# Kernel optimization log

Hardware: AMD Instinct MI355X
Metric: run time of the kernel (lower is better)

Reference implementation:

```python
import jax, jax.numpy as jnp
import numpy as np

N_EMBD = 1024
N_HEAD = 16
HEAD_SIZE = N_EMBD // N_HEAD  # 64
EPS = 1e-5


def layer_norm(x, gamma, beta):
    mu = jnp.mean(x, axis=-1, keepdims=True)
    var = jnp.var(x, axis=-1, keepdims=True)
    return (x - mu) * jax.lax.rsqrt(var + EPS) * gamma + beta


def setup_inputs() -> dict:
    key = jax.random.key(0)
    ks = jax.random.split(key, 12)
    B, T, C, H, hs = 4, 2048, N_EMBD, N_HEAD, HEAD_SIZE
    s = 0.02
    return {
        "x": jax.random.normal(ks[0], (B, T, C), jnp.float32),
        # per-head projections, stacked over heads: [H, C, hs]
        "Wq": jax.random.normal(ks[1], (H, C, hs), jnp.float32) * s,
        "Wk": jax.random.normal(ks[2], (H, C, hs), jnp.float32) * s,
        "Wv": jax.random.normal(ks[3], (H, C, hs), jnp.float32) * s,
        "Wo": jax.random.normal(ks[4], (C, C), jnp.float32) * s,
        "bo": jnp.zeros((C,), jnp.float32),
        "W1": jax.random.normal(ks[5], (C, 4 * C), jnp.float32) * s,
        "b1": jnp.zeros((4 * C,), jnp.float32),
        "W2": jax.random.normal(ks[6], (4 * C, C), jnp.float32) * s,
        "b2": jnp.zeros((C,), jnp.float32),
        "g1": jnp.ones((C,), jnp.float32),
        "be1": jnp.zeros((C,), jnp.float32),
        "g2": jnp.ones((C,), jnp.float32),
        "be2": jnp.zeros((C,), jnp.float32),
    }


def reference(x, Wq, Wk, Wv, Wo, bo, W1, b1, W2, b2, g1, be1, g2, be2):
    B, T, C = x.shape
    # --- self-attention branch (pre-LN) ---
    h = layer_norm(x, g1, be1)
    q = jnp.einsum("btc,hcd->bhtd", h, Wq)
    k = jnp.einsum("btc,hcd->bhtd", h, Wk)
    v = jnp.einsum("btc,hcd->bhtd", h, Wv)
    scale = HEAD_SIZE ** -0.5
    wei = jnp.einsum("bhtd,bhsd->bhts", q, k) * scale  # [B,H,T,T]
    causal = jnp.tril(jnp.ones((T, T), bool))
    wei = jnp.where(causal, wei, -jnp.inf)
    wei = jax.nn.softmax(wei, axis=-1)
    attn = jnp.einsum("bhts,bhsd->bhtd", wei, v)  # [B,H,T,hs]
    # concat heads -> [B,T,C]
    attn = attn.transpose(0, 2, 1, 3).reshape(B, T, C)
    x = x + attn @ Wo + bo
    # --- MLP branch (pre-LN) ---
    h = layer_norm(x, g2, be2)
    h = jax.nn.relu(h @ W1 + b1) @ W2 + b2
    return x + h
```

## Files before the change

### kernel.cpp

```cpp
#include <hip/hip_runtime.h>
#include <cstdint>
#include <cstddef>


typedef unsigned short u16;
typedef __attribute__((ext_vector_type(8))) __bf16 bf16x8;
typedef __attribute__((ext_vector_type(4))) short s16x4;
typedef __attribute__((ext_vector_type(4))) float f32x4;

#if defined(__has_builtin)
#if __has_builtin(__builtin_amdgcn_global_load_lds)
#define HAS_GLL 1
#endif
#endif

#define QSCALE 0.18033688011112042f

__device__ __forceinline__ u16 f2bf(float f) {
  union { float f; unsigned int u; } c; c.f = f;
  unsigned int u = c.u;
  u += 0x7FFFu + ((u >> 16) & 1u);
  return (u16)(u >> 16);
}
__device__ __forceinline__ u16 f2bf_fast(float f) {
  union { float f; unsigned int u; } c; c.f = f;
  return (u16)((c.u + 0x8000u) >> 16);
}

__device__ __forceinline__ float fexp2(float x) {
#if defined(__HIP_DEVICE_COMPILE__)
#if defined(__has_builtin) && __has_builtin(__builtin_amdgcn_exp2f)
  return __builtin_amdgcn_exp2f(x);
#else
  float r;
  asm("v_exp_f32 %0, %1" : "=v"(r) : "v"(x));
  return r;
#endif
#else
  return x;
#endif
}

__device__ __forceinline__ f32x4 mfma_pv(s16x4 a, s16x4 b, f32x4 c) {
#if defined(__HIP_DEVICE_COMPILE__)
#if defined(__has_builtin) && __has_builtin(__builtin_amdgcn_mfma_f32_16x16x16bf16_1k)
  return __builtin_amdgcn_mfma_f32_16x16x16bf16_1k(a, b, c, 0, 0, 0);
#else
  f32x4 d;
  asm volatile("v_mfma_f32_16x16x16_bf16 %0, %1, %2, %3"
               : "=v"(d) : "v"(a), "v"(b), "v"(c));
  return d;
#endif
#else
  (void)a; (void)b;
  return c;
#endif
}

__device__ __forceinline__ void stage16(const u16* g, u16* l, int lane) {
#ifdef HAS_GLL
  __builtin_amdgcn_global_load_lds(
      (const __attribute__((address_space(1))) uint32_t*)(g),
      (__attribute__((address_space(3))) uint32_t*)(l), 16, 0, 0);
#else
  *(int4*)(l + lane * 8) = *(const int4*)g;
#endif
}

__global__ __launch_bounds__(256) void ln_k(const float* __restrict__ x,
                                            const float* __restrict__ g,
                                            const float* __restrict__ be,
                                            u16* __restrict__ out) {
  const int row = blockIdx.x;
  const int t = threadIdx.x;
  const float4 v = ((const float4*)(x + (size_t)row * 1024))[t];
  float s = v.x + v.y + v.z + v.w;
  float s2 = v.x * v.x + v.y * v.y + v.z * v.z + v.w * v.w;
#pragma unroll
  for (int off = 32; off > 0; off >>= 1) {
    s += __shfl_down(s, off);
    s2 += __shfl_down(s2, off);
  }
  __shared__ float red[8];
  if ((t & 63) == 0) { red[t >> 6] = s; red[4 + (t >> 6)] = s2; }
  __syncthreads();
  const float ts = red[0] + red[1] + red[2] + red[3];
  const float ts2 = red[4] + red[5] + red[6] + red[7];
  const float mu = ts * (1.0f / 1024.0f);
  const float var = ts2 * (1.0f / 1024.0f) - mu * mu;
  const float rstd = rsqrtf(var + 1e-5f);
  const float4 gv = ((const float4*)g)[t];
  const float4 bv = ((const float4*)be)[t];
  u16* op = out + (size_t)row * 1024 + t * 4;
  op[0] = f2bf((v.x - mu) * rstd * gv.x + bv.x);
  op[1] = f2bf((v.y - mu) * rstd * gv.y + bv.y);
  op[2] = f2bf((v.z - mu) * rstd * gv.z + bv.z);
  op[3] = f2bf((v.w - mu) * rstd * gv.w + bv.w);
}

__global__ __launch_bounds__(256) void transpose_k(const float* __restrict__ in,
                                                   u16* __restrict__ out,
                                                   int R, int Cc) {
  __shared__ float tile[32][33];
  const size_t base = (size_t)blockIdx.z * R * Cc;
  const int r0 = blockIdx.x * 32, c0 = blockIdx.y * 32;
  const int tx = threadIdx.x & 31, ty = threadIdx.x >> 5;
  const float* ip = in + base;
  u16* op = out + base;
#pragma unroll
  for (int i = 0; i < 32; i += 8)
    tile[ty + i][tx] = ip[(size_t)(r0 + ty + i) * Cc + c0 + tx];
  __syncthreads();
#pragma unroll
  for (int i = 0; i < 32; i += 8)
    op[(size_t)(c0 + ty + i) * R + r0 + tx] = f2bf(tile[tx][ty + i]);
}

template <int MODE>
__global__ __launch_bounds__(256, 2) void gemm_k(
    const u16* __restrict__ A, const u16* __restrict__ Bt,
    const float* __restrict__ bias, const float* __restrict__ resid,
    void* __restrict__ out0, void* __restrict__ out1, void* __restrict__ out2,
    int M, int N, int K) {
  __shared__ u16 As[2][2][128 * 32];
  __shared__ u16 Bs[2][2][128 * 32];
  const int tid = threadIdx.x;
  const int lane = tid & 63;
  const int w = tid >> 6;
  const int wm = w & 1, wn = w >> 1;
  const int l15 = lane & 15, lq = lane >> 4;
  const int m0 = blockIdx.x * 128, n0 = blockIdx.y * 128;
  const int srow = lane >> 2, scol = (lane & 3) * 8;

  f32x4 acc[4][4] = {};

  const u16* gA0 = A  + (size_t)(m0 + w * 32 + srow) * K + scol;
  const u16* gA1 = gA0 + (size_t)16 * K;
  const u16* gB0 = Bt + (size_t)(n0 + w * 32 + srow) * K + scol;
  const u16* gB1 = gB0 + (size_t)16 * K;
  const int lofs = (w * 32) * 32;

  auto STAGE = [&](int buf, int k0) {
    stage16(gA0 + k0,      &As[buf][0][lofs], lane);
    stage16(gA1 + k0,      &As[buf][0][lofs + 512], lane);
    stage16(gA0 + k0 + 32, &As[buf][1][lofs], lane);
    stage16(gA1 + k0 + 32, &As[buf][1][lofs + 512], lane);
    stage16(gB0 + k0,      &Bs[buf][0][lofs], lane);
    stage16(gB1 + k0,      &Bs[buf][0][lofs + 512], lane);
    stage16(gB0 + k0 + 32, &Bs[buf][1][lofs], lane);
    stage16(gB1 + k0 + 32, &Bs[buf][1][lofs + 512], lane);
  };

  STAGE(0, 0);

  int cur = 0;
  for (int k0 = 0; k0 < K; k0 += 64) {
    if (k0 + 64 < K) {
      STAGE(cur ^ 1, k0 + 64);
      asm volatile("s_waitcnt vmcnt(8)" ::: "memory");
    } else {
      asm volatile("s_waitcnt vmcnt(0)" ::: "memory");
    }
    __builtin_amdgcn_s_barrier();
    __builtin_amdgcn_sched_barrier(0);
#pragma unroll
    for (int kk = 0; kk < 2; ++kk) {
      bf16x8 af[4], bfr[4];
#pragma unroll
      for (int i = 0; i < 4; ++i)
        af[i] = *(const bf16x8*)&As[cur][kk][(wm * 64 + i * 16 + l15) * 32 + lq * 8];
#pragma unroll
      for (int j = 0; j < 4; ++j)
        bfr[j] = *(const bf16x8*)&Bs[cur][kk][(wn * 64 + j * 16 + l15) * 32 + lq * 8];
#pragma unroll
      for (int i = 0; i < 4; ++i)
#pragma unroll
        for (int j = 0; j < 4; ++j)
          acc[i][j] = __builtin_amdgcn_mfma_f32_16x16x32_bf16(af[i], bfr[j], acc[i][j], 0, 0, 0);
    }
    __builtin_amdgcn_sched_barrier(0);
    __builtin_amdgcn_s_barrier();
    cur ^= 1;
  }

#pragma unroll
  for (int i = 0; i < 4; ++i) {
    const int mbase = m0 + wm * 64 + i * 16 + lq * 4;
#pragma unroll
    for (int j = 0; j < 4; ++j) {
      const int ncol = n0 + wn * 64 + j * 16 + l15;
#pragma unroll
      for (int r = 0; r < 4; ++r) {
        const float v = acc[i][j][r];
        const int m = mbase + r;
        if (MODE == 0) {
          const int which = ncol >> 10;
          const int hh = (ncol >> 6) & 15;
          const int dd = ncol & 63;
          const int tt = m & 2047;
          const size_t bhb = (size_t)((m >> 11) * 16 + hh) * 131072;
          if (which == 0) {
            ((u16*)out0)[bhb + tt * 64 + dd] = f2bf(v * QSCALE);
          } else if (which == 1) {
            ((u16*)out1)[bhb + (tt >> 4) * 1024 + (dd >> 5) * 512 +
                         ((((dd & 31) >> 3) * 16 + (tt & 15)) << 3) + (dd & 7)] = f2bf(v);
          } else {
            ((u16*)out2)[bhb + (dd >> 4) * 32768 + (tt >> 4) * 256 +
                         (((dd & 15) + (((tt >> 2) & 3)) * 16) << 2) + (tt & 3)] = f2bf(v);
          }
        } else if (MODE == 1 || MODE == 3) {
          ((float*)out0)[(size_t)m * N + ncol] =
              v + bias[ncol] + resid[(size_t)m * N + ncol];
        } else {
          const float t2 = v + bias[ncol];
          ((u16*)out0)[(size_t)m * N + ncol] = f2bf(t2 > 0.0f ? t2 : 0.0f);
        }
      }
    }
  }
}

__global__ __launch_bounds__(256, 4) void flash_k(const u16* __restrict__ q,
                                                  const u16* __restrict__ k,
                                                  const u16* __restrict__ vt,
                                                  u16* __restrict__ attn) {
  const int bh = blockIdx.x;
  const int qblk = 15 - blockIdx.y;
  const int bb = bh >> 4, hh = bh & 15;
  const int tid = threadIdx.x;
  const int lane = tid & 63, wid = tid >> 6;
  const int l15 = lane & 15, lq = lane >> 4;
  const int q0w = qblk * 128 + wid * 32;

  const u16* qrowA = q + ((size_t)bh * 2048 + q0w + l15) * 64 + lq * 8;
  const bf16x8 qA0 = *(const bf16x8*)qrowA;
  const bf16x8 qA1 = *(const bf16x8*)(qrowA + 32);
  const u16* qrowB = qrowA + 16 * 64;
  const bf16x8 qB0 = *(const bf16x8*)qrowB;
  const bf16x8 qB1 = *(const bf16x8*)(qrowB + 32);

  const u16* kC = k + (size_t)bh * 131072 + lane * 8;
  const u16* vC = vt + (size_t)bh * 131072 + lane * 4;

  f32x4 oA[4] = {}, oB[4] = {};
  float lA = 0.0f, lB = 0.0f;

  const int nt = q0w >> 4;

#pragma unroll 2
  for (int t = 0; t < nt; ++t) {
    const int ko = t * 1024, vo = t * 256;
    const bf16x8 ck0 = *(const bf16x8*)(kC + ko);
    const bf16x8 ck1 = *(const bf16x8*)(kC + ko + 512);
    const s16x4 cv0 = *(const s16x4*)(vC + vo);
    const s16x4 cv1 = *(const s16x4*)(vC + vo + 32768);
    const s16x4 cv2 = *(const s16x4*)(vC + vo + 65536);
    const s16x4 cv3 = *(const s16x4*)(vC + vo + 98304);

    f32x4 stA = {}, stB = {};
    __builtin_amdgcn_s_setprio(1);
    stA = __builtin_amdgcn_mfma_f32_16x16x32_bf16(ck0, qA0, stA, 0, 0, 0);
    stA = __builtin_amdgcn_mfma_f32_16x16x32_bf16(ck1, qA1, stA, 0, 0, 0);
    stB = __builtin_amdgcn_mfma_f32_16x16x32_bf16(ck0, qB0, stB, 0, 0, 0);
    stB = __builtin_amdgcn_mfma_f32_16x16x32_bf16(ck1, qB1, stB, 0, 0, 0);
    __builtin_amdgcn_s_setprio(0);

    const float a0 = fexp2(stA[0]), a1 = fexp2(stA[1]);
    const float a2 = fexp2(stA[2]), a3 = fexp2(stA[3]);
    const float b0 = fexp2(stB[0]), b1 = fexp2(stB[1]);
    const float b2 = fexp2(stB[2]), b3 = fexp2(stB[3]);
    lA += (a0 + a1) + (a2 + a3);
    lB += (b0 + b1) + (b2 + b3);
    s16x4 pfA, pfB;
    pfA[0] = (short)f2bf_fast(a0); pfA[1] = (short)f2bf_fast(a1);
    pfA[2] = (short)f2bf_fast(a2); pfA[3] = (short)f2bf_fast(a3);
    pfB[0] = (short)f2bf_fast(b0); pfB[1] = (short)f2bf_fast(b1);
    pfB[2] = (short)f2bf_fast(b2); pfB[3] = (short)f2bf_fast(b3);

    __builtin_amdgcn_s_setprio(1);
    oA[0] = mfma_pv(cv0, pfA, oA[0]);
    oA[1] = mfma_pv(cv1, pfA, oA[1]);
    oA[2] = mfma_pv(cv2, pfA, oA[2]);
    oA[3] = mfma_pv(cv3, pfA, oA[3]);
    oB[0] = mfma_pv(cv0, pfB, oB[0]);
    oB[1] = mfma_pv(cv1, pfB, oB[1]);
    oB[2] = mfma_pv(cv2, pfB, oB[2]);
    oB[3] = mfma_pv(cv3, pfB, oB[3]);
    __builtin_amdgcn_s_setprio(0);
  }

  {
    const int ko = nt * 1024, vo = nt * 256;
    const bf16x8 ck0 = *(const bf16x8*)(kC + ko);
    const bf16x8 ck1 = *(const bf16x8*)(kC + ko + 512);
    const s16x4 cv0 = *(const s16x4*)(vC + vo);
    const s16x4 cv1 = *(const s16x4*)(vC + vo + 32768);
    const s16x4 cv2 = *(const s16x4*)(vC + vo + 65536);
    const s16x4 cv3 = *(const s16x4*)(vC + vo + 98304);

    f32x4 stA = {}, stB = {};
    stA = __builtin_amdgcn_mfma_f32_16x16x32_bf16(ck0, qA0, stA, 0, 0, 0);
    stA = __builtin_amdgcn_mfma_f32_16x16x32_bf16(ck1, qA1, stA, 0, 0, 0);
    stB = __builtin_amdgcn_mfma_f32_16x16x32_bf16(ck0, qB0, stB, 0, 0, 0);
    stB = __builtin_amdgcn_mfma_f32_16x16x32_bf16(ck1, qB1, stB, 0, 0, 0);
#pragma unroll
    for (int r = 0; r < 4; ++r)
      if (lq * 4 + r > l15) stA[r] = -1e30f;

    const float a0 = fexp2(stA[0]), a1 = fexp2(stA[1]);
    const float a2 = fexp2(stA[2]), a3 = fexp2(stA[3]);
    const float b0 = fexp2(stB[0]), b1 = fexp2(stB[1]);
    const float b2 = fexp2(stB[2]), b3 = fexp2(stB[3]);
    lA += (a0 + a1) + (a2 + a3);
    lB += (b0 + b1) + (b2 + b3);
    s16x4 pfA, pfB;
    pfA[0] = (short)f2bf_fast(a0); pfA[1] = (short)f2bf_fast(a1);
    pfA[2] = (short)f2bf_fast(a2); pfA[3] = (short)f2bf_fast(a3);
    pfB[0] = (short)f2bf_fast(b0); pfB[1] = (short)f2bf_fast(b1);
    pfB[2] = (short)f2bf_fast(b2); pfB[3] = (short)f2bf_fast(b3);

    oA[0] = mfma_pv(cv0, pfA, oA[0]);
    oA[1] = mfma_pv(cv1, pfA, oA[1]);
    oA[2] = mfma_pv(cv2, pfA, oA[2]);
    oA[3] = mfma_pv(cv3, pfA, oA[3]);
    oB[0] = mfma_pv(cv0, pfB, oB[0]);
    oB[1] = mfma_pv(cv1, pfB, oB[1]);
    oB[2] = mfma_pv(cv2, pfB, oB[2]);
    oB[3] = mfma_pv(cv3, pfB, oB[3]);
  }

  {
    const int ko = (nt + 1) * 1024, vo = (nt + 1) * 256;
    const bf16x8 ck0 = *(const bf16x8*)(kC + ko);
    const bf16x8 ck1 = *(const bf16x8*)(kC + ko + 512);
    const s16x4 cv0 = *(const s16x4*)(vC + vo);
    const s16x4 cv1 = *(const s16x4*)(vC + vo + 32768);
    const s16x4 cv2 = *(const s16x4*)(vC + vo + 65536);
    const s16x4 cv3 = *(const s16x4*)(vC + vo + 98304);

    f32x4 stB = {};
    stB = __builtin_amdgcn_mfma_f32_16x16x32_bf16(ck0, qB0, stB, 0, 0, 0);
    stB = __builtin_amdgcn_mfma_f32_16x16x32_bf16(ck1, qB1, stB, 0, 0, 0);
#pragma unroll
    for (int r = 0; r < 4; ++r)
      if (lq * 4 + r > l15) stB[r] = -1e30f;

    const float b0 = fexp2(stB[0]), b1 = fexp2(stB[1]);
    const float b2 = fexp2(stB[2]), b3 = fexp2(stB[3]);
    lB += (b0 + b1) + (b2 + b3);
    s16x4 pfB;
    pfB[0] = (short)f2bf_fast(b0); pfB[1] = (short)f2bf_fast(b1);
    pfB[2] = (short)f2bf_fast(b2); pfB[3] = (short)f2bf_fast(b3);

    oB[0] = mfma_pv(cv0, pfB, oB[0]);
    oB[1] = mfma_pv(cv1, pfB, oB[1]);
    oB[2] = mfma_pv(cv2, pfB, oB[2]);
    oB[3] = mfma_pv(cv3, pfB, oB[3]);
  }

  lA += __shfl_xor(lA, 16);
  lA += __shfl_xor(lA, 32);
  lB += __shfl_xor(lB, 16);
  lB += __shfl_xor(lB, 32);
  const float rlA = 1.0f / lA;
  const float rlB = 1.0f / lB;

  u16* opA = attn + ((size_t)bb * 2048 + q0w + l15) * 1024 + hh * 64 + lq * 4;
  u16* opB = opA + 16 * 1024;
#pragma unroll
  for (int dt = 0; dt < 4; ++dt) {
    union { s16x4 v; u16 a[4]; } pk;
#pragma unroll
    for (int r = 0; r < 4; ++r) pk.a[r] = f2bf(oA[dt][r] * rlA);
    *(s16x4*)(opA + dt * 16) = pk.v;
#pragma unroll
    for (int r = 0; r < 4; ++r) pk.a[r] = f2bf(oB[dt][r] * rlB);
    *(s16x4*)(opB + dt * 16) = pk.v;
  }
}

extern "C" void kernel_launch(void* const* d_in, const int* in_sizes, int n_in,
                              void* d_out, int out_size, void* d_ws, size_t ws_size,
                              hipStream_t stream) {
  const float* x   = (const float*)d_in[0];
  const float* Wq  = (const float*)d_in[1];
  const float* Wk  = (const float*)d_in[2];
  const float* Wv  = (const float*)d_in[3];
  const float* Wo  = (const float*)d_in[4];
  const float* bo  = (const float*)d_in[5];
  const float* W1  = (const float*)d_in[6];
  const float* b1  = (const float*)d_in[7];
  const float* W2  = (const float*)d_in[8];
  const float* b2  = (const float*)d_in[9];
  const float* g1  = (const float*)d_in[10];
  const float* be1 = (const float*)d_in[11];
  const float* g2  = (const float*)d_in[12];
  const float* be2 = (const float*)d_in[13];
  float* out = (float*)d_out;

  char* ws = (char*)d_ws;
  u16* Wqkv_t = (u16*)(ws + 0);
  u16* Wo_t   = (u16*)(ws + 6291456);
  u16* W1_t   = (u16*)(ws + 8388608);
  u16* W2_t   = (u16*)(ws + 16777216);
  u16* hbuf   = (u16*)(ws + 25165824);
  float* x2   = (float*)(ws + 41943040);
  u16* vtb    = (u16*)(ws + 41943040);
  u16* qb     = (u16*)(ws + 75497472);
  u16* kb     = (u16*)(ws + 92274688);
  u16* attnb  = (u16*)(ws + 109051904);
  u16* a1     = (u16*)(ws + 75497472);

  dim3 blk(256);

  transpose_k<<<dim3(32, 2, 16),  blk, 0, stream>>>(Wq, Wqkv_t,            1024, 64);
  transpose_k<<<dim3(32, 2, 16),  blk, 0, stream>>>(Wk, Wqkv_t + 1048576,  1024, 64);
  transpose_k<<<dim3(32, 2, 16),  blk, 0, stream>>>(Wv, Wqkv_t + 2097152,  1024, 64);
  transpose_k<<<dim3(32, 32, 1),  blk, 0, stream>>>(Wo, Wo_t,              1024, 1024);
  transpose_k<<<dim3(32, 128, 1), blk, 0, stream>>>(W1, W1_t,              1024, 4096);
  transpose_k<<<dim3(128, 32, 1), blk, 0, stream>>>(W2, W2_t,              4096, 1024);

  ln_k<<<8192, blk, 0, stream>>>(x, g1, be1, hbuf);
  gemm_k<0><<<dim3(64, 24), blk, 0, stream>>>(hbuf, Wqkv_t, nullptr, nullptr,
                                              qb, kb, vtb, 8192, 3072, 1024);
  flash_k<<<dim3(64, 16), blk, 0, stream>>>(qb, kb, vtb, attnb);
  gemm_k<1><<<dim3(64, 8), blk, 0, stream>>>(attnb, Wo_t, bo, x,
                                             x2, nullptr, nullptr, 8192, 1024, 1024);
  ln_k<<<8192, blk, 0, stream>>>(x2, g2, be2, hbuf);
  gemm_k<2><<<dim3(64, 32), blk, 0, stream>>>(hbuf, W1_t, b1, nullptr,
                                              a1, nullptr, nullptr, 8192, 4096, 1024);
  gemm_k<3><<<dim3(64, 8), blk, 0, stream>>>(a1, W2_t, b2, x2,
                                             out, nullptr, nullptr, 8192, 1024, 4096);
}
```

Measured before the change: 493.1 us.

## Switch GEMM to triple-buffered 32-wide K stages with higher occupancy

The GEMM mainloop now uses three 32-wide K shared-memory buffers instead of two 64-wide double buffers, prefetching two stages ahead. Shared memory per block shrinks, and launch bounds are raised to three blocks per CU. This aims to hide global-load latency better and raise occupancy. In exchange there are twice as many barriers per K, less MFMA work between synchronisations, and a tighter register budget that could cause spills.

Result: slower. 508.3 us (+3.1%).

```diff
diff --git a/kernel.cpp b/kernel.cpp
--- a/kernel.cpp
+++ b/kernel.cpp
@@ -117,13 +117,13 @@
 }
 
 template <int MODE>
-__global__ __launch_bounds__(256, 2) void gemm_k(
+__global__ __launch_bounds__(256, 3) void gemm_k(
     const u16* __restrict__ A, const u16* __restrict__ Bt,
     const float* __restrict__ bias, const float* __restrict__ resid,
     void* __restrict__ out0, void* __restrict__ out1, void* __restrict__ out2,
     int M, int N, int K) {
-  __shared__ u16 As[2][2][128 * 32];
-  __shared__ u16 Bs[2][2][128 * 32];
+  __shared__ u16 As[3][128 * 32];
+  __shared__ u16 Bs[3][128 * 32];
   const int tid = threadIdx.x;
   const int lane = tid & 63;
   const int w = tid >> 6;
@@ -141,46 +141,43 @@
   const int lofs = (w * 32) * 32;
 
   auto STAGE = [&](int buf, int k0) {
-    stage16(gA0 + k0,      &As[buf][0][lofs], lane);
-    stage16(gA1 + k0,      &As[buf][0][lofs + 512], lane);
-    stage16(gA0 + k0 + 32, &As[buf][1][lofs], lane);
-    stage16(gA1 + k0 + 32, &As[buf][1][lofs + 512], lane);
-    stage16(gB0 + k0,      &Bs[buf][0][lofs], lane);
-    stage16(gB1 + k0,      &Bs[buf][0][lofs + 512], lane);
-    stage16(gB0 + k0 + 32, &Bs[buf][1][lofs], lane);
-    stage16(gB1 + k0 + 32, &Bs[buf][1][lofs + 512], lane);
+    stage16(gA0 + k0, &As[buf][lofs], lane);
+    stage16(gA1 + k0, &As[buf][lofs + 512], lane);
+    stage16(gB0 + k0, &Bs[buf][lofs], lane);
+    stage16(gB1 + k0, &Bs[buf][lofs + 512], lane);
   };
 
   STAGE(0, 0);
-
-  int cur = 0;
-  for (int k0 = 0; k0 < K; k0 += 64) {
-    if (k0 + 64 < K) {
-      STAGE(cur ^ 1, k0 + 64);
+  STAGE(1, 32);
+
+  int cur = 0, stg = 2;
+  for (int k0 = 0; k0 < K; k0 += 32) {
+    if (k0 + 96 <= K) {
+      STAGE(stg, k0 + 64);
       asm volatile("s_waitcnt vmcnt(8)" ::: "memory");
+    } else if (k0 + 64 == K) {
+      asm volatile("s_waitcnt vmcnt(4)" ::: "memory");
     } else {
       asm volatile("s_waitcnt vmcnt(0)" ::: "memory");
     }
     __builtin_amdgcn_s_barrier();
     __builtin_amdgcn_sched_barrier(0);
-#pragma unroll
-    for (int kk = 0; kk < 2; ++kk) {
-      bf16x8 af[4], bfr[4];
-#pragma unroll
-      for (int i = 0; i < 4; ++i)
-        af[i] = *(const bf16x8*)&As[cur][kk][(wm * 64 + i * 16 + l15) * 32 + lq * 8];
+    bf16x8 af[4], bfr[4];
+#pragma unroll
+    for (int i = 0; i < 4; ++i)
+      af[i] = *(const bf16x8*)&As[cur][(wm * 64 + i * 16 + l15) * 32 + lq * 8];
+#pragma unroll
+    for (int j = 0; j < 4; ++j)
+      bfr[j] = *(const bf16x8*)&Bs[cur][(wn * 64 + j * 16 + l15) * 32 + lq * 8];
+#pragma unroll
+    for (int i = 0; i < 4; ++i)
 #pragma unroll
       for (int j = 0; j < 4; ++j)
-        bfr[j] = *(const bf16x8*)&Bs[cur][kk][(wn * 64 + j * 16 + l15) * 32 + lq * 8];
-#pragma unroll
-      for (int i = 0; i < 4; ++i)
-#pragma unroll
-        for (int j = 0; j < 4; ++j)
-          acc[i][j] = __builtin_amdgcn_mfma_f32_16x16x32_bf16(af[i], bfr[j], acc[i][j], 0, 0, 0);
-    }
+        acc[i][j] = __builtin_amdgcn_mfma_f32_16x16x32_bf16(af[i], bfr[j], acc[i][j], 0, 0, 0);
     __builtin_amdgcn_sched_barrier(0);
     __builtin_amdgcn_s_barrier();
-    cur ^= 1;
+    cur = (cur == 2) ? 0 : cur + 1;
+    stg = (stg == 2) ? 0 : stg + 1;
   }
 
 #pragma unroll
```
